# Performance work log

Hardware: AMD Instinct MI355X
Metric: run time of the kernel (lower is better)

Reference implementation:

```python
import jax, jax.numpy as jnp
import numpy as np

B, M, N = 16, 64, 64
F = 64
H2 = 2 * F
L = 2
OUT1, OUT2, PREDS = 32, 32, 256


def skew(x):
    # (b,m,n,c) -> (b,m,m+n-1,c); row i shifted right by i
    b, m, n, c = x.shape
    pad = jnp.pad(x, ((0, 0), (0, 0), (0, m - 1), (0, 0)))
    return jax.vmap(lambda row, r: jnp.roll(row, r, axis=1), in_axes=(1, 0), out_axes=1)(pad, jnp.arange(m))


def unskew(x):
    b, m, n2, c = x.shape
    n = n2 - m + 1
    un = jax.vmap(lambda row, r: jnp.roll(row, -r, axis=1), in_axes=(1, 0), out_axes=1)(x, jnp.arange(m))
    return un[:, :, :n]


def _ln(x, s, b, eps=1e-6):
    mu = jnp.mean(x, axis=-1, keepdims=True)
    var = jnp.mean(jnp.square(x - mu), axis=-1, keepdims=True)
    return (x - mu) * jax.lax.rsqrt(var + eps) * s + b


def _diag_layer(xin, lns, lnb, wis, bis, wss, bss, woc, boc, h0p):
    # xin: (b,m,n2,2F); scan over diagonals (n2 axis)
    b, m, n2, h2 = xin.shape
    f = h2 // 2

    def step(carry, xt):  # xt: (b,m,2F)
        h, c = carry
        xn = _ln(xt, lns, lnb)
        # is_kernel: 1x1 conv == linear; ss_kernel: causal k=2 conv along m
        hprev = jnp.pad(h, ((0, 0), (1, 0), (0, 0)))[:, :-1]
        z = xn @ wis + bis + hprev @ wss[0] + h @ wss[1] + bss  # (b,m,4F)
        fg, ig, og, gg = jnp.split(z, 4, axis=-1)
        cn = jax.nn.sigmoid(fg) * c + jax.nn.sigmoid(ig) * jnp.tanh(gg)
        hn = jax.nn.sigmoid(og) * jnp.tanh(cn)
        x_out = hn @ woc + boc + xn  # residual uses post-LN x (as in source)
        return (hn, cn), x_out

    h0t = jnp.broadcast_to(h0p, (b, m, f))  # h0p: (1,F)
    c0 = jnp.zeros((b, m, f), xin.dtype)
    _, out = jax.lax.scan(step, (h0t, c0), xin.transpose(2, 0, 1, 3))
    return out.transpose(1, 2, 0, 3)


def _forward(im, conv_in_k, conv_in_b, ln_s, ln_b, w_is, b_is, w_ss, b_ss,
             w_oc, b_oc, h0, w_out1, b_out1, w_out2, b_out2, w_head, b_head):
    # mask-A for the 7x7 input conv
    mask = jnp.ones(conv_in_k.shape, conv_in_k.dtype)
    mask = mask.at[3:, 4:].set(0.0)
    mask = mask.at[4:].set(0.0)
    mask = mask.at[3, 3].set(0.0)
    x = skew(im)  # (b,m,n2,1)
    x = jax.lax.conv_general_dilated(x, conv_in_k * mask, (1, 1), 'SAME',
                                     dimension_numbers=('NHWC', 'HWIO', 'NHWC')) + conv_in_b
    b, m, n2, h2 = x.shape
    for l in range(ln_s.shape[0]):
        left = _diag_layer(x, ln_s[l, 0], ln_b[l, 0], w_is[l, 0], b_is[l, 0],
                           w_ss[l, 0], b_ss[l, 0], w_oc[l, 0], b_oc[l, 0], h0[l, 0])
        right = _diag_layer(x[:, :, ::-1, :], ln_s[l, 1], ln_b[l, 1], w_is[l, 1], b_is[l, 1],
                            w_ss[l, 1], b_ss[l, 1], w_oc[l, 1], b_oc[l, 1], h0[l, 1])[:, :, ::-1, :]
        right = jnp.concatenate([jnp.zeros((b, 1, n2, h2), x.dtype), right[:, :-1]], axis=1)
        x = left + right
    x = unskew(x)  # (b,m,n,2F)
    x = x @ w_out1 + b_out1
    x = x @ w_out2 + b_out2
    return x @ w_head + b_head  # (b,m,n,256)


def setup_inputs() -> dict:
    key = jax.random.key(0)
    ks = jax.random.split(key, 10)
    rn = lambda k, s: jax.random.normal(k, s, jnp.float32) * 0.05
    return {
        "im": jax.random.uniform(ks[0], (B, M, N, 1), jnp.float32),
        "conv_in_k": rn(ks[1], (7, 7, 1, H2)),
        "conv_in_b": jnp.zeros((H2,), jnp.float32),
        "ln_s": jnp.ones((L, 2, H2), jnp.float32),
        "ln_b": jnp.zeros((L, 2, H2), jnp.float32),
        "w_is": rn(ks[2], (L, 2, H2, 4 * F)),
        "b_is": jnp.zeros((L, 2, 4 * F), jnp.float32),
        "w_ss": rn(ks[3], (L, 2, 2, F, 4 * F)),
        "b_ss": jnp.zeros((L, 2, 4 * F), jnp.float32),
        "w_oc": rn(ks[4], (L, 2, F, H2)),
        "b_oc": jnp.zeros((L, 2, H2), jnp.float32),
        "h0": rn(ks[5], (L, 2, 1, F)),
        "w_out1": rn(ks[6], (H2, OUT1)),
        "b_out1": jnp.zeros((OUT1,), jnp.float32),
        "w_out2": rn(ks[7], (OUT1, OUT2)),
        "b_out2": jnp.zeros((OUT2,), jnp.float32),
        "w_head": rn(ks[8], (OUT2, PREDS)),
        "b_head": jnp.zeros((PREDS,), jnp.float32),
    }


def reference(im, conv_in_k, conv_in_b, ln_s, ln_b, w_is, b_is, w_ss, b_ss,
              w_oc, b_oc, h0, w_out1, b_out1, w_out2, b_out2, w_head, b_head):
    return _forward(im, conv_in_k, conv_in_b, ln_s, ln_b, w_is, b_is, w_ss, b_ss,
                    w_oc, b_oc, h0, w_out1, b_out1, w_out2, b_out2, w_head, b_head)
```

## Files before the change

### kernel.cpp

```cpp
#include <hip/hip_runtime.h>

typedef unsigned short ushort_t;
typedef unsigned int uint_t;
typedef __attribute__((ext_vector_type(8))) short s8bf;
typedef __attribute__((ext_vector_type(4))) float f32x4;

#define N2 127
#define ACT ((size_t)16*64*127*128)
#define HNE ((size_t)16*64*127*64)
#define MBW ((size_t)32*3*127*64)

__device__ inline float bf_lo(uint_t v){ return __uint_as_float(v << 16); }
__device__ inline float bf_hi(uint_t v){ return __uint_as_float(v & 0xffff0000u); }
__device__ inline ushort_t f2bf(float f){
  uint_t u = __float_as_uint(f);
  uint_t r = ((u >> 16) & 1u) + 0x7fffu;
  return (ushort_t)((u + r) >> 16);
}
__device__ inline uint_t cvt_pk_bf16(float lo, float hi){
  uint_t r;
  asm("v_cvt_pk_bf16_f32 %0, %1, %2" : "=v"(r) : "v"(lo), "v"(hi));
  return r;
}
__device__ inline float bf2f(ushort_t h){ return __uint_as_float(((uint_t)h) << 16); }
__device__ inline float frcp(float x){ return __builtin_amdgcn_rcpf(x); }
__device__ inline float sigm(float x){ return frcp(1.f + __expf(-x)); }
__device__ inline float tanhf_(float x){
  float e = __expf(2.f * x);
  return 1.f - 2.f * frcp(1.f + e);
}
__device__ inline void unpack8(uint4 u, float* x){
  x[0]=bf_lo(u.x); x[1]=bf_hi(u.x); x[2]=bf_lo(u.y); x[3]=bf_hi(u.y);
  x[4]=bf_lo(u.z); x[5]=bf_hi(u.z); x[6]=bf_lo(u.w); x[7]=bf_hi(u.w);
}
__device__ inline f32x4 zero4(){ f32x4 v; v[0]=0.f; v[1]=0.f; v[2]=0.f; v[3]=0.f; return v; }
__device__ inline f32x4 splat4(float s){ f32x4 v; v[0]=s; v[1]=s; v[2]=s; v[3]=s; return v; }

__device__ inline void rowstats16(const float* xr, float& mu, float& rstd){
  float s0=0.f, q0=0.f;
#pragma unroll
  for (int k = 0; k < 16; k++){ s0 += xr[k]; q0 += xr[k]*xr[k]; }
  s0 += __shfl_xor(s0, 1); q0 += __shfl_xor(q0, 1);
  s0 += __shfl_xor(s0, 2); q0 += __shfl_xor(q0, 2);
  s0 += __shfl_xor(s0, 4); q0 += __shfl_xor(q0, 4);
  mu = s0 * 0.0078125f;
  float var = q0 * 0.0078125f - mu*mu;
  rstd = rsqrtf(var + 1e-6f);
}

__global__ __launch_bounds__(256) void prep_kernel(
    const float* __restrict__ im, const float* __restrict__ cb,
    const float* __restrict__ ck,
    const float* __restrict__ w_is, const float* __restrict__ w_ss,
    const float* __restrict__ b_is, const float* __restrict__ b_ss,
    const float* __restrict__ w_oc, const float* __restrict__ w1,
    const float* __restrict__ w2, const float* __restrict__ wh,
    ushort_t* __restrict__ out,
    ushort_t* __restrict__ zWp, ushort_t* __restrict__ wisp,
    ushort_t* __restrict__ wocp,
    float* __restrict__ zbias, float* __restrict__ w1T,
    float* __restrict__ w2T, float* __restrict__ whT,
    uint_t* __restrict__ mb)
{
  __shared__ float ims[4][64];
  const int tid = threadIdx.x;

  if (blockIdx.x < 1024){
    const int b = blockIdx.x >> 6;
    const int i = blockIdx.x & 63;
    {
      int r = tid >> 6, c = tid & 63;
      int ii = i - 3 + r;
      ims[r][c] = (ii >= 0) ? im[(b*64 + ii)*64 + c] : 0.f;
    }
    const int ch = tid & 127;
    const int jh = tid >> 7;
    float kwreg[24];
#pragma unroll
    for (int tau = 0; tau < 24; tau++){
      int di = (tau < 21) ? (tau/7 - 3) : 0;
      int dj = (tau < 21) ? (tau%7 - 3) : (tau - 24);
      kwreg[tau] = ck[((di+3)*7 + (dj+3))*128 + ch];
    }
    const float cbv = cb[ch];
    __syncthreads();
    ushort_t* orow = out + ((size_t)(b*64 + i)*N2)*128 + ch;
#pragma unroll 1
    for (int jt = 0; jt < 64; jt++){
      int j = jt*2 + jh;
      if (j >= N2) break;
      int base = j - i;
      float acc = cbv;
#pragma unroll
      for (int tau = 0; tau < 24; tau++){
        int di = (tau < 21) ? (tau/7 - 3) : 0;
        int dj = (tau < 21) ? (tau%7 - 3) : (tau - 24);
        int jx = base + dj - di;
        int r = di + 3;
        if (jx >= 0 && jx < 64)
          acc += ims[r][jx] * kwreg[tau];
      }
      orow[(size_t)j*128] = f2bf(acc);
    }
    return;
  }

  int idx = (blockIdx.x - 1024) * 256 + tid;
  if (idx < 131072){
    int ld = idx >> 15; int r = idx & 32767;
    int e = r & 7, lane = (r >> 3) & 63, ctg = (r >> 9) & 15, kk = r >> 13;
    int k = kk*32 + ((lane >> 4) & 3)*8 + e;
    int n = ctg*16 + (lane & 15);
    float v;
    if (k < 64) v = w_ss[(((size_t)ld*2 + 0)*64 + k)*256 + n];
    else        v = w_ss[(((size_t)ld*2 + 1)*64 + (k-64))*256 + n];
    zWp[idx] = f2bf(v);
  } else if (idx < 262144){
    int r0 = idx - 131072;
    int ld = r0 >> 15; int r = r0 & 32767;
    int e = r & 7, lane = (r >> 3) & 63, ctg = (r >> 9) & 15, kk = r >> 13;
    int k = kk*32 + ((lane >> 4) & 3)*8 + e;
    int n = ctg*16 + (lane & 15);
    wisp[r0] = f2bf(w_is[((size_t)ld*128 + k)*256 + n]);
  } else if (idx < 294912){
    int r0 = idx - 262144;
    int ld = r0 >> 13; int r = r0 & 8191;
    int e = r & 7, lane = (r >> 3) & 63, ctg = (r >> 9) & 7, kk = (r >> 12) & 1;
    int k = kk*32 + ((lane >> 4) & 3)*8 + e;
    int n = ctg*16 + (lane & 15);
    wocp[r0] = f2bf(w_oc[((size_t)ld*64 + k)*128 + n]);
  } else if (idx < 295936){
    int r = idx - 294912;
    zbias[r] = b_is[r] + b_ss[r];
  } else if (idx < 300032){
    int r = idx - 295936;
    int c = r >> 7, k = r & 127;
    w1T[r] = w1[k*32 + c];
  } else if (idx < 301056){
    int r = idx - 300032;
    int c = r >> 5, k = r & 31;
    w2T[r] = w2[k*32 + c];
  } else if (idx < 309248){
    int r = idx - 301056;
    int o = r >> 5, k = r & 31;
    whT[r] = wh[k*256 + o];
  } else if (idx >= 312320 && idx < (int)(312320 + MBW/4)){
    ((uint4*)mb)[idx - 312320] = make_uint4(0u, 0u, 0u, 0u);
  }
}

__device__ inline void write_frags512(const ushort_t* __restrict__ XN,
                                      ushort_t* __restrict__ dst, int tid){
  int lane = tid & 63, t8 = tid >> 6;
  int quad = (lane >> 4) & 3, l16 = lane & 15;
  int kk = t8 >> 1, rh = (t8 & 1)*2;
#pragma unroll
  for (int i = 0; i < 2; i++){
    int rt = rh + i;
    uint4 v = *(const uint4*)&XN[(size_t)(rt*16 + l16)*136 + kk*32 + quad*8];
    *(uint4*)(dst + (size_t)((kk*4 + rt)*64 + lane)*8) = v;
  }
}

__device__ inline void ln_to_XN16(ushort_t* __restrict__ XN, int row, int lq,
                                  const float* xr, float mu, float rstd,
                                  const float* __restrict__ ln_s,
                                  const float* __restrict__ ln_b, int ld){
  uint_t o[8];
#pragma unroll
  for (int k2 = 0; k2 < 8; k2++){
    int c = lq*16 + 2*k2;
    float a = (xr[2*k2]   - mu)*rstd*ln_s[ld*128 + c]     + ln_b[ld*128 + c];
    float b = (xr[2*k2+1] - mu)*rstd*ln_s[ld*128 + c + 1] + ln_b[ld*128 + c + 1];
    o[k2] = cvt_pk_bf16(a, b);
  }
  uint4* dst = (uint4*)&XN[(size_t)row*136 + lq*16];
  dst[0] = make_uint4(o[0], o[1], o[2], o[3]);
  dst[1] = make_uint4(o[4], o[5], o[6], o[7]);
}

__global__ __launch_bounds__(512) void stage0_kernel(
    int lnlyr, const ushort_t* __restrict__ Xbuf,
    const float* __restrict__ ln_s, const float* __restrict__ ln_b,
    ushort_t* __restrict__ xnfL, ushort_t* __restrict__ xnfR)
{
  __shared__ __align__(16) ushort_t XN[64*136];

  const int tid = threadIdx.x;
  const int bj = blockIdx.x;
  const int b = bj / 127, j = bj - b*127;
  const int row = tid >> 3, lq = tid & 7;

  float xr[16];
  {
    const uint4* p = (const uint4*)(Xbuf + ((size_t)(b*64 + row)*N2 + j)*128 + lq*16);
    unpack8(p[0], xr); unpack8(p[1], xr+8);
  }
  float mu, rstd;
  rowstats16(xr, mu, rstd);

  ln_to_XN16(XN, row, lq, xr, mu, rstd, ln_s, ln_b, lnlyr*2 + 0);
  __syncthreads();
  write_frags512(XN, xnfL + (size_t)bj*8192, tid);
  __syncthreads();
  ln_to_XN16(XN, row, lq, xr, mu, rstd, ln_s, ln_b, lnlyr*2 + 1);
  __syncthreads();
  write_frags512(XN, xnfR + (size_t)bj*8192, tid);
}

__global__ __launch_bounds__(512, 1) void stage12_kernel(
    int mode, int woclyr, int lnlyr,
    ushort_t* __restrict__ Xbuf,
    const ushort_t* __restrict__ hnL, const ushort_t* __restrict__ hnR,
    const ushort_t* __restrict__ wocp, const float* __restrict__ b_oc,
    const float* __restrict__ ln_s, const float* __restrict__ ln_b,
    ushort_t* __restrict__ xnfL, ushort_t* __restrict__ xnfR)
{
  __shared__ __align__(16) float Xout[64*132];
  __shared__ __align__(16) ushort_t XN[64*136];
  __shared__ __align__(16) ushort_t XNh[64*72];

  const int tid = threadIdx.x;
  const int bj = blockIdx.x;
  const int b = bj / 127, j = bj - b*127;
  const int w8 = tid >> 6;
  const int lane = tid & 63, quad = (lane >> 4) & 3, l16 = lane & 15;
  const int row = tid >> 3, lq = tid & 7;

  float xr[16];
  {
    const uint4* p = (const uint4*)(Xbuf + ((size_t)(b*64 + row)*N2 + j)*128 + lq*16);
    unpack8(p[0], xr); unpack8(p[1], xr+8);
  }
  float mu, rstd;
  rowstats16(xr, mu, rstd);

#pragma unroll 1
  for (int s = 0; s < 2; s++){
    const int ld = woclyr*2 + s;
    ln_to_XN16(XN, row, lq, xr, mu, rstd, ln_s, ln_b, ld);
    {
      const ushort_t* hp = s ? hnR : hnL;
      const uint4* p = (const uint4*)(hp + ((size_t)(b*64 + row)*N2 + j)*64 + lq*8);
      *(uint4*)&XNh[(size_t)row*72 + lq*8] = p[0];
    }
    __syncthreads();
    s8bf bw[2];
#pragma unroll
    for (int kk = 0; kk < 2; kk++)
      bw[kk] = *(const s8bf*)(wocp + (size_t)ld*8192 + (size_t)(((kk*8 + w8)*64 + lane)*8));
    f32x4 a2[4];
#pragma unroll
    for (int rt = 0; rt < 4; rt++) a2[rt] = zero4();
#pragma unroll
    for (int kk = 0; kk < 2; kk++)
#pragma unroll
      for (int rt = 0; rt < 4; rt++){
        s8bf a = *(const s8bf*)&XNh[(size_t)(rt*16 + l16)*72 + kk*32 + quad*8];
        a2[rt] = __builtin_amdgcn_mfma_f32_16x16x32_bf16(a, bw[kk], a2[rt], 0, 0, 0);
      }
    const float bv = b_oc[ld*128 + w8*16 + l16];
    const int col = w8*16 + l16;
#pragma unroll
    for (int rt = 0; rt < 4; rt++)
#pragma unroll
      for (int r = 0; r < 4; r++){
        int rr = rt*16 + quad*4 + r;
        float v = a2[rt][r] + bv + bf2f(XN[(size_t)rr*136 + col]);
        if (s == 0) Xout[(size_t)rr*132 + col] = v;
        else if (rr < 63) Xout[(size_t)(rr + 1)*132 + col] += v;
      }
    __syncthreads();
  }

  float xo[16];
#pragma unroll
  for (int k = 0; k < 16; k++) xo[k] = Xout[(size_t)row*132 + lq*16 + k];
  {
    uint_t o[8];
#pragma unroll
    for (int k = 0; k < 8; k++) o[k] = cvt_pk_bf16(xo[2*k], xo[2*k + 1]);
    uint4* dst = (uint4*)(Xbuf + ((size_t)(b*64 + row)*N2 + j)*128 + lq*16);
    dst[0] = make_uint4(o[0], o[1], o[2], o[3]);
    dst[1] = make_uint4(o[4], o[5], o[6], o[7]);
  }
  if (mode == 2) return;

  float mu2, rstd2;
  rowstats16(xo, mu2, rstd2);
  ln_to_XN16(XN, row, lq, xo, mu2, rstd2, ln_s, ln_b, lnlyr*2 + 0);
  __syncthreads();
  write_frags512(XN, xnfL + (size_t)bj*8192, tid);
  __syncthreads();
  ln_to_XN16(XN, row, lq, xo, mu2, rstd2, ln_s, ln_b, lnlyr*2 + 1);
  __syncthreads();
  write_frags512(XN, xnfR + (size_t)bj*8192, tid);
}

__global__ __launch_bounds__(256, 1) void diag_kernel(
    const ushort_t* __restrict__ xnfL, const ushort_t* __restrict__ xnfR,
    ushort_t* __restrict__ hnL, ushort_t* __restrict__ hnR,
    const ushort_t* __restrict__ zWp, const ushort_t* __restrict__ wisp,
    const float* __restrict__ zbias, const float* __restrict__ h0, int layer,
    uint_t* __restrict__ mb)
{
  __shared__ ushort_t A[2][16][136];

  const int tid = threadIdx.x;
  const int g = blockIdx.x & 3;
  const int b = (blockIdx.x >> 2) & 15;
  const int d = blockIdx.x >> 6;
  const int ld = layer*2 + d;
  const ushort_t* xnf = d ? xnfR : xnfL;
  ushort_t* hp = d ? hnR : hnL;

  const int w = tid >> 6;
  const int lane = tid & 63;
  const int quad = lane >> 4;
  const int l16 = lane & 15;
  const int cg = w*16 + l16;

  s8bf bss[4][4], bis[4][4];
#pragma unroll
  for (int kk = 0; kk < 4; kk++)
#pragma unroll
    for (int ct = 0; ct < 4; ct++){
      size_t fo = (size_t)(((kk*16 + (w + 4*ct))*64 + lane)*8);
      bss[kk][ct] = *(const s8bf*)(zWp  + (size_t)ld*32768 + fo);
      bis[kk][ct] = *(const s8bf*)(wisp + (size_t)ld*32768 + fo);
    }
  float zb[4];
#pragma unroll
  for (int ct = 0; ct < 4; ct++) zb[ct] = zbias[ld*256 + ct*64 + cg];

  float c_reg[4] = {0.f, 0.f, 0.f, 0.f};

  {
    int r2 = tid >> 4, q8 = tid & 15;
    const float* h0p = h0 + ld*64;
#pragma unroll
    for (int k = 0; k < 8; k++){
      int c = q8*8 + k;
      ushort_t hb = f2bf(h0p[c & 63]);
      ushort_t v;
      if (c < 64) v = (g == 0 && r2 == 0) ? (ushort_t)0 : hb;
      else        v = hb;
      A[0][r2][c] = v;
      A[1][r2][c] = v;
    }
  }

  const int stp8 = d ? -8192 : 8192;
  const ushort_t* xbase = xnf + ((size_t)b*127 + (d ? 126 : 0))*8192;
  uint4 xf[4];
#pragma unroll
  for (int kk = 0; kk < 4; kk++)
    xf[kk] = *(const uint4*)(xbase + (size_t)((kk*4 + g)*64 + lane)*8);

  f32x4 acc[4];
#pragma unroll
  for (int ct = 0; ct < 4; ct++) acc[ct] = splat4(zb[ct]);
#pragma unroll
  for (int kk = 0; kk < 4; kk++){
    s8bf a = *(const s8bf*)&xf[kk];
#pragma unroll
    for (int ct = 0; ct < 4; ct++)
      acc[ct] = __builtin_amdgcn_mfma_f32_16x16x32_bf16(a, bis[kk][ct], acc[ct], 0, 0, 0);
  }
  const ushort_t* pfp = xbase + stp8;
#pragma unroll
  for (int kk = 0; kk < 4; kk++)
    xf[kk] = *(const uint4*)(pfp + (size_t)((kk*4 + g)*64 + lane)*8);
  pfp += stp8;

  const int dj64 = d ? -64 : 64;
  ushort_t* hlane = hp + ((size_t)(b*64 + g*16 + quad*4)*N2 + (d ? 126 : 0))*64 + cg;

  const int bd = b*2 + d;
  uint_t* mbOut = mb + ((size_t)(bd*3 + g)*127)*64;
  const uint_t* mbIn = mb + ((size_t)(bd*3 + (g > 0 ? g - 1 : 0))*127)*64;
  const uint_t stampBase = (uint_t)layer * 127u;
  const bool isProd = (g < 3);
  const bool isCons = (g > 0) && (w == 1);

  __syncthreads();

#pragma unroll 1
  for (int t = 0; t < 127; t++){
    const int pr = t & 1, pn = pr ^ 1;
    const uint_t stamp = stampBase + (uint_t)t + 1u;
    const bool doFetch = isCons && (t < 126);

    uint_t pv = 0;
    if (doFetch)
      pv = __hip_atomic_load(mbIn + (size_t)t*64 + lane,
                             __ATOMIC_RELAXED, __HIP_MEMORY_SCOPE_AGENT);

#pragma unroll
    for (int kk = 0; kk < 4; kk++){
      s8bf af = *(const s8bf*)&A[pr][l16][kk*32 + quad*8];
#pragma unroll
      for (int ct = 0; ct < 4; ct++)
        acc[ct] = __builtin_amdgcn_mfma_f32_16x16x32_bf16(af, bss[kk][ct], acc[ct], 0, 0, 0);
    }

#pragma unroll
    for (int r = 0; r < 4; r++){
      float fg = sigm(acc[0][r]);
      float ig = sigm(acc[1][r]);
      float og = sigm(acc[2][r]);
      float gg = tanhf_(acc[3][r]);
      float cn = fg*c_reg[r] + ig*gg;
      c_reg[r] = cn;
      float hn = og * tanhf_(cn);
      int rr = quad*4 + r;
      ushort_t hb = f2bf(hn);
      A[pn][rr][64 + cg] = hb;
      if (rr < 15) A[pn][rr + 1][cg] = hb;
      hlane[(size_t)r*8128] = hb;
      if (r == 3 && isProd && quad == 3 && t < 126)
        __hip_atomic_store(mbOut + (size_t)t*64 + cg,
                           (stamp << 16) | (uint_t)hb,
                           __ATOMIC_RELAXED, __HIP_MEMORY_SCOPE_AGENT);
    }
    hlane += dj64;

    if (t < 126){
#pragma unroll
      for (int ct = 0; ct < 4; ct++) acc[ct] = splat4(zb[ct]);
#pragma unroll
      for (int kk = 0; kk < 4; kk++){
        s8bf a = *(const s8bf*)&xf[kk];
#pragma unroll
        for (int ct = 0; ct < 4; ct++)
          acc[ct] = __builtin_amdgcn_mfma_f32_16x16x32_bf16(a, bis[kk][ct], acc[ct], 0, 0, 0);
      }
      if (t < 125){
#pragma unroll
        for (int kk = 0; kk < 4; kk++)
          xf[kk] = *(const uint4*)(pfp + (size_t)((kk*4 + g)*64 + lane)*8);
        pfp += stp8;
      }
    }

    if (doFetch){
      while (!__all((pv >> 16) == stamp))
        pv = __hip_atomic_load(mbIn + (size_t)t*64 + lane,
                               __ATOMIC_RELAXED, __HIP_MEMORY_SCOPE_AGENT);
      A[pn][0][lane] = (ushort_t)(pv & 0xffffu);
    }

    __syncthreads();
  }
}

__global__ __launch_bounds__(512) void head_kernel(
    const ushort_t* __restrict__ xfin,
    const float* __restrict__ w1T, const float* __restrict__ b1,
    const float* __restrict__ w2T, const float* __restrict__ b2,
    const float* __restrict__ whT, const float* __restrict__ bh,
    float* __restrict__ out)
{
  __shared__ float xf[64][132];
  __shared__ float v1[64][36];
  __shared__ float v2[64][36];
  int tid = threadIdx.x;
  int b = blockIdx.x >> 6, i = blockIdx.x & 63;
  {
    int jj = tid >> 3, q = tid & 7;
    size_t base = ((size_t)(b*64 + i)*N2 + (i + jj))*128 + q*16;
    const uint4* pL = (const uint4*)(xfin + base);
    float x[16];
    unpack8(pL[0], x); unpack8(pL[1], x+8);
#pragma unroll
    for (int k = 0; k < 16; k++) xf[jj][q*16 + k] = x[k];
  }
  __syncthreads();
  {
    int c1 = tid & 31, jg = tid >> 5;
    float accv[4];
#pragma unroll
    for (int q = 0; q < 4; q++) accv[q] = b1[c1];
#pragma unroll 1
    for (int kc = 0; kc < 4; kc++){
      float wr[32];
      const float4* wp = (const float4*)(w1T + c1*128 + kc*32);
#pragma unroll
      for (int kk = 0; kk < 8; kk++) ((float4*)wr)[kk] = wp[kk];
#pragma unroll
      for (int jj2 = 0; jj2 < 4; jj2++){
        int jr = jg*4 + jj2;
        float a0=0.f,a1=0.f,a2=0.f,a3=0.f;
#pragma unroll
        for (int kk = 0; kk < 8; kk++){
          float4 xv = *(const float4*)&xf[jr][kc*32 + kk*4];
          a0 += xv.x*wr[kk*4]; a1 += xv.y*wr[kk*4+1]; a2 += xv.z*wr[kk*4+2]; a3 += xv.w*wr[kk*4+3];
        }
        accv[jj2] += (a0+a1)+(a2+a3);
      }
    }
#pragma unroll
    for (int jj2 = 0; jj2 < 4; jj2++) v1[jg*4 + jj2][c1] = accv[jj2];
  }
  __syncthreads();
  {
    int c2 = tid & 31, jg = tid >> 5;
    float wr[32];
    const float4* wp = (const float4*)(w2T + c2*32);
#pragma unroll
    for (int kk = 0; kk < 8; kk++) ((float4*)wr)[kk] = wp[kk];
#pragma unroll
    for (int jj2 = 0; jj2 < 4; jj2++){
      int jr = jg*4 + jj2;
      float a0=0.f,a1=0.f,a2=0.f,a3=0.f;
#pragma unroll
      for (int kk = 0; kk < 8; kk++){
        float4 xv = *(const float4*)&v1[jr][kk*4];
        a0 += xv.x*wr[kk*4]; a1 += xv.y*wr[kk*4+1]; a2 += xv.z*wr[kk*4+2]; a3 += xv.w*wr[kk*4+3];
      }
      v2[jr][c2] = b2[c2] + (a0+a1)+(a2+a3);
    }
  }
  __syncthreads();
  {
    int o = tid & 255, jh = tid >> 8;
    float wr[32];
    const float4* wp = (const float4*)(whT + o*32);
#pragma unroll
    for (int kk = 0; kk < 8; kk++) ((float4*)wr)[kk] = wp[kk];
    float bo = bh[o];
#pragma unroll 1
    for (int jr2 = 0; jr2 < 32; jr2++){
      int jr = jh*32 + jr2;
      float a0=0.f,a1=0.f,a2=0.f,a3=0.f;
#pragma unroll
      for (int kk = 0; kk < 8; kk++){
        float4 xv = *(const float4*)&v2[jr][kk*4];
        a0 += xv.x*wr[kk*4]; a1 += xv.y*wr[kk*4+1]; a2 += xv.z*wr[kk*4+2]; a3 += xv.w*wr[kk*4+3];
      }
      out[(((size_t)b*64 + i)*64 + jr)*256 + o] = bo + (a0+a1)+(a2+a3);
    }
  }
}

extern "C" void kernel_launch(void* const* d_in, const int* in_sizes, int n_in,
                              void* d_out, int out_size, void* d_ws, size_t ws_size,
                              hipStream_t stream)
{
  const float* im   = (const float*)d_in[0];
  const float* ck   = (const float*)d_in[1];
  const float* cb   = (const float*)d_in[2];
  const float* ln_s = (const float*)d_in[3];
  const float* ln_b = (const float*)d_in[4];
  const float* w_is = (const float*)d_in[5];
  const float* b_is = (const float*)d_in[6];
  const float* w_ss = (const float*)d_in[7];
  const float* b_ss = (const float*)d_in[8];
  const float* w_oc = (const float*)d_in[9];
  const float* b_oc = (const float*)d_in[10];
  const float* h0   = (const float*)d_in[11];
  const float* w1   = (const float*)d_in[12];
  const float* b1   = (const float*)d_in[13];
  const float* w2   = (const float*)d_in[14];
  const float* b2   = (const float*)d_in[15];
  const float* wh   = (const float*)d_in[16];
  const float* bh   = (const float*)d_in[17];

  ushort_t* Xbuf = (ushort_t*)d_ws;
  ushort_t* xnfL = Xbuf + ACT;
  ushort_t* xnfR = xnfL + ACT;
  ushort_t* hnL  = xnfR + ACT;
  ushort_t* hnR  = hnL + HNE;
  ushort_t* zWp  = hnR + HNE;
  ushort_t* wisp = zWp + 131072;
  ushort_t* wocp = wisp + 131072;
  float* zbias = (float*)(wocp + 32768);
  float* w1T   = zbias + 1024;
  float* w2T   = w1T + 4096;
  float* whT   = w2T + 1024;
  uint_t* mb   = (uint_t*)d_out;

  prep_kernel<<<3006, 256, 0, stream>>>(im, cb, ck, w_is, w_ss, b_is, b_ss,
                                        w_oc, w1, w2, wh, Xbuf,
                                        zWp, wisp, wocp, zbias, w1T, w2T, whT, mb);
  stage0_kernel<<<2032, 512, 0, stream>>>(0, Xbuf, ln_s, ln_b, xnfL, xnfR);
  diag_kernel<<<128, 256, 0, stream>>>(xnfL, xnfR, hnL, hnR, zWp, wisp, zbias, h0, 0, mb);
  stage12_kernel<<<2032, 512, 0, stream>>>(1, 0, 1, Xbuf, hnL, hnR,
                                           wocp, b_oc, ln_s, ln_b, xnfL, xnfR);
  diag_kernel<<<128, 256, 0, stream>>>(xnfL, xnfR, hnL, hnR, zWp, wisp, zbias, h0, 1, mb);
  stage12_kernel<<<2032, 512, 0, stream>>>(2, 1, 0, Xbuf, hnL, hnR,
                                           wocp, b_oc, ln_s, ln_b, xnfL, xnfR);
  head_kernel<<<1024, 512, 0, stream>>>(Xbuf, w1T, b1, w2T, b2, whT, bh, (float*)d_out);
}
```

Baseline: 655.0 us.

## Fuse stage and diagonal kernels with per-column flags to overlap producer and scan

Merges the LN/fragment producer kernels with the diagonal LSTM scan kernel into single launches. The first 128 blocks run the scan and spin on per-(batch,diagonal) flags that producer blocks set after writing fragments with agent-scope stores. The aim is to overlap the serial diagonal scan with the parallel stage work and cut kernel launch gaps. It risks deadlock if the scan blocks occupy CUs the producers need, adds spin-wait overhead, and doubles the hn buffers so layer-0 outputs stay intact while layer 1 runs.

```diff
diff --git a/kernel.cpp b/kernel.cpp
--- a/kernel.cpp
+++ b/kernel.cpp
@@ -60,7 +60,7 @@
     ushort_t* __restrict__ wocp,
     float* __restrict__ zbias, float* __restrict__ w1T,
     float* __restrict__ w2T, float* __restrict__ whT,
-    uint_t* __restrict__ mb)
+    uint_t* __restrict__ flg, uint_t* __restrict__ mb)
 {
   __shared__ float ims[4][64];
   const int tid = threadIdx.x;
@@ -144,8 +144,27 @@
     int r = idx - 301056;
     int o = r >> 5, k = r & 31;
     whT[r] = wh[k*256 + o];
+  } else if (idx < 311280){
+    flg[idx - 309248] = 0u;
   } else if (idx >= 312320 && idx < (int)(312320 + MBW/4)){
     ((uint4*)mb)[idx - 312320] = make_uint4(0u, 0u, 0u, 0u);
+  }
+}
+
+__device__ inline void write_frags512A(const ushort_t* __restrict__ XN,
+                                       ushort_t* __restrict__ dst, int tid){
+  int lane = tid & 63, t8 = tid >> 6;
+  int quad = (lane >> 4) & 3, l16 = lane & 15;
+  int kk = t8 >> 1, rh = (t8 & 1)*2;
+#pragma unroll
+  for (int i = 0; i < 2; i++){
+    int rt = rh + i;
+    uint4 v = *(const uint4*)&XN[(size_t)(rt*16 + l16)*136 + kk*32 + quad*8];
+    uint_t* d = (uint_t*)(dst + (size_t)((kk*4 + rt)*64 + lane)*8);
+    __hip_atomic_store(d+0, v.x, __ATOMIC_RELAXED, __HIP_MEMORY_SCOPE_AGENT);
+    __hip_atomic_store(d+1, v.y, __ATOMIC_RELAXED, __HIP_MEMORY_SCOPE_AGENT);
+    __hip_atomic_store(d+2, v.z, __ATOMIC_RELAXED, __HIP_MEMORY_SCOPE_AGENT);
+    __hip_atomic_store(d+3, v.w, __ATOMIC_RELAXED, __HIP_MEMORY_SCOPE_AGENT);
   }
 }
 
@@ -179,15 +198,12 @@
   dst[1] = make_uint4(o[4], o[5], o[6], o[7]);
 }
 
-__global__ __launch_bounds__(512) void stage0_kernel(
-    int lnlyr, const ushort_t* __restrict__ Xbuf,
+__device__ void stage0_body(int bj, int tid, const ushort_t* __restrict__ Xbuf,
     const float* __restrict__ ln_s, const float* __restrict__ ln_b,
-    ushort_t* __restrict__ xnfL, ushort_t* __restrict__ xnfR)
-{
-  __shared__ __align__(16) ushort_t XN[64*136];
-
-  const int tid = threadIdx.x;
-  const int bj = blockIdx.x;
+    ushort_t* __restrict__ xnfL, ushort_t* __restrict__ xnfR,
+    uint_t* __restrict__ flg, uint_t fstamp, char* smem)
+{
+  ushort_t* XN = (ushort_t*)smem;
   const int b = bj / 127, j = bj - b*127;
   const int row = tid >> 3, lq = tid & 7;
 
@@ -199,29 +215,31 @@
   float mu, rstd;
   rowstats16(xr, mu, rstd);
 
-  ln_to_XN16(XN, row, lq, xr, mu, rstd, ln_s, ln_b, lnlyr*2 + 0);
-  __syncthreads();
-  write_frags512(XN, xnfL + (size_t)bj*8192, tid);
-  __syncthreads();
-  ln_to_XN16(XN, row, lq, xr, mu, rstd, ln_s, ln_b, lnlyr*2 + 1);
-  __syncthreads();
-  write_frags512(XN, xnfR + (size_t)bj*8192, tid);
-}
-
-__global__ __launch_bounds__(512, 1) void stage12_kernel(
-    int mode, int woclyr, int lnlyr,
+  ln_to_XN16(XN, row, lq, xr, mu, rstd, ln_s, ln_b, 0);
+  __syncthreads();
+  write_frags512A(XN, xnfL + (size_t)bj*8192, tid);
+  __syncthreads();
+  ln_to_XN16(XN, row, lq, xr, mu, rstd, ln_s, ln_b, 1);
+  __syncthreads();
+  write_frags512A(XN, xnfR + (size_t)bj*8192, tid);
+  asm volatile("s_waitcnt vmcnt(0)" ::: "memory");
+  __syncthreads();
+  if (tid == 0)
+    __hip_atomic_store(&flg[bj], fstamp, __ATOMIC_RELAXED, __HIP_MEMORY_SCOPE_AGENT);
+}
+
+__device__ void stage12_body(int bj, int tid, int mode, int woclyr, int lnlyr,
     ushort_t* __restrict__ Xbuf,
     const ushort_t* __restrict__ hnL, const ushort_t* __restrict__ hnR,
     const ushort_t* __restrict__ wocp, const float* __restrict__ b_oc,
     const float* __restrict__ ln_s, const float* __restrict__ ln_b,
-    ushort_t* __restrict__ xnfL, ushort_t* __restrict__ xnfR)
-{
-  __shared__ __align__(16) float Xout[64*132];
-  __shared__ __align__(16) ushort_t XN[64*136];
-  __shared__ __align__(16) ushort_t XNh[64*72];
-
-  const int tid = threadIdx.x;
-  const int bj = blockIdx.x;
+    ushort_t* __restrict__ xnfL, ushort_t* __restrict__ xnfR,
+    uint_t* __restrict__ flg, uint_t fstamp, char* smem)
+{
+  float* Xout  = (float*)smem;
+  ushort_t* XN = (ushort_t*)(smem + 33792);
+  ushort_t* XNh= (ushort_t*)(smem + 51200);
+
   const int b = bj / 127, j = bj - b*127;
   const int w8 = tid >> 6;
   const int lane = tid & 63, quad = (lane >> 4) & 3, l16 = lane & 15;
@@ -290,26 +308,28 @@
   rowstats16(xo, mu2, rstd2);
   ln_to_XN16(XN, row, lq, xo, mu2, rstd2, ln_s, ln_b, lnlyr*2 + 0);
   __syncthreads();
-  write_frags512(XN, xnfL + (size_t)bj*8192, tid);
+  write_frags512A(XN, xnfL + (size_t)bj*8192, tid);
   __syncthreads();
   ln_to_XN16(XN, row, lq, xo, mu2, rstd2, ln_s, ln_b, lnlyr*2 + 1);
   __syncthreads();
-  write_frags512(XN, xnfR + (size_t)bj*8192, tid);
-}
-
-__global__ __launch_bounds__(256, 1) void diag_kernel(
+  write_frags512A(XN, xnfR + (size_t)bj*8192, tid);
+  asm volatile("s_waitcnt vmcnt(0)" ::: "memory");
+  __syncthreads();
+  if (tid == 0)
+    __hip_atomic_store(&flg[bj], fstamp, __ATOMIC_RELAXED, __HIP_MEMORY_SCOPE_AGENT);
+}
+
+__device__ void diag_body(int blk, int tid,
     const ushort_t* __restrict__ xnfL, const ushort_t* __restrict__ xnfR,
     ushort_t* __restrict__ hnL, ushort_t* __restrict__ hnR,
     const ushort_t* __restrict__ zWp, const ushort_t* __restrict__ wisp,
     const float* __restrict__ zbias, const float* __restrict__ h0, int layer,
-    uint_t* __restrict__ mb)
-{
-  __shared__ ushort_t A[2][16][136];
-
-  const int tid = threadIdx.x;
-  const int g = blockIdx.x & 3;
-  const int b = (blockIdx.x >> 2) & 15;
-  const int d = blockIdx.x >> 6;
+    uint_t* __restrict__ mb, const uint_t* __restrict__ flg, uint_t fstamp,
+    ushort_t* __restrict__ Ap )
+{
+  const int g = blk & 3;
+  const int b = (blk >> 2) & 15;
+  const int d = blk >> 6;
   const int ld = layer*2 + d;
   const ushort_t* xnf = d ? xnfR : xnfL;
   ushort_t* hp = d ? hnR : hnL;
@@ -345,13 +365,20 @@
       ushort_t v;
       if (c < 64) v = (g == 0 && r2 == 0) ? (ushort_t)0 : hb;
       else        v = hb;
-      A[0][r2][c] = v;
-      A[1][r2][c] = v;
+      Ap[(0*16 + r2)*136 + c] = v;
+      Ap[(1*16 + r2)*136 + c] = v;
     }
   }
 
   const int stp8 = d ? -8192 : 8192;
   const ushort_t* xbase = xnf + ((size_t)b*127 + (d ? 126 : 0))*8192;
+  const uint_t* fbase = flg + b*127;
+
+  {
+    const uint_t* f0 = fbase + (d ? 126 : 0);
+    while (__hip_atomic_load(f0, __ATOMIC_RELAXED, __HIP_MEMORY_SCOPE_AGENT) < fstamp) {}
+    asm volatile("" ::: "memory");
+  }
   uint4 xf[4];
 #pragma unroll
   for (int kk = 0; kk < 4; kk++)
@@ -366,12 +393,19 @@
 #pragma unroll
     for (int ct = 0; ct < 4; ct++)
       acc[ct] = __builtin_amdgcn_mfma_f32_16x16x32_bf16(a, bis[kk][ct], acc[ct], 0, 0, 0);
+  }
+  {
+    const uint_t* f1 = fbase + (d ? 125 : 1);
+    while (__hip_atomic_load(f1, __ATOMIC_RELAXED, __HIP_MEMORY_SCOPE_AGENT) < fstamp) {}
+    asm volatile("" ::: "memory");
   }
   const ushort_t* pfp = xbase + stp8;
 #pragma unroll
   for (int kk = 0; kk < 4; kk++)
     xf[kk] = *(const uint4*)(pfp + (size_t)((kk*4 + g)*64 + lane)*8);
   pfp += stp8;
+  const uint_t* fpf = fbase + (d ? 124 : 2);
+  const int fstep = d ? -1 : 1;
 
   const int dj64 = d ? -64 : 64;
   ushort_t* hlane = hp + ((size_t)(b*64 + g*16 + quad*4)*N2 + (d ? 126 : 0))*64 + cg;
@@ -395,10 +429,13 @@
     if (doFetch)
       pv = __hip_atomic_load(mbIn + (size_t)t*64 + lane,
                              __ATOMIC_RELAXED, __HIP_MEMORY_SCOPE_AGENT);
+    uint_t fv = 0xffffffffu;
+    if (t < 125)
+      fv = __hip_atomic_load(fpf, __ATOMIC_RELAXED, __HIP_MEMORY_SCOPE_AGENT);
 
 #pragma unroll
     for (int kk = 0; kk < 4; kk++){
-      s8bf af = *(const s8bf*)&A[pr][l16][kk*32 + quad*8];
+      s8bf af = *(const s8bf*)&Ap[(pr*16 + l16)*136 + kk*32 + quad*8];
 #pragma unroll
       for (int ct = 0; ct < 4; ct++)
         acc[ct] = __builtin_amdgcn_mfma_f32_16x16x32_bf16(af, bss[kk][ct], acc[ct], 0, 0, 0);
@@ -415,8 +452,8 @@
       float hn = og * tanhf_(cn);
       int rr = quad*4 + r;
       ushort_t hb = f2bf(hn);
-      A[pn][rr][64 + cg] = hb;
-      if (rr < 15) A[pn][rr + 1][cg] = hb;
+      Ap[(pn*16 + rr)*136 + 64 + cg] = hb;
+      if (rr < 15) Ap[(pn*16 + rr + 1)*136 + cg] = hb;
       hlane[(size_t)r*8128] = hb;
       if (r == 3 && isProd && quad == 3 && t < 126)
         __hip_atomic_store(mbOut + (size_t)t*64 + cg,
@@ -436,10 +473,15 @@
           acc[ct] = __builtin_amdgcn_mfma_f32_16x16x32_bf16(a, bis[kk][ct], acc[ct], 0, 0, 0);
       }
       if (t < 125){
+        if (fv < fstamp){
+          while (__hip_atomic_load(fpf, __ATOMIC_RELAXED, __HIP_MEMORY_SCOPE_AGENT) < fstamp) {}
+        }
+        asm volatile("" ::: "memory");
 #pragma unroll
         for (int kk = 0; kk < 4; kk++)
           xf[kk] = *(const uint4*)(pfp + (size_t)((kk*4 + g)*64 + lane)*8);
         pfp += stp8;
+        fpf += fstep;
       }
     }
 
@@ -447,11 +489,72 @@
       while (!__all((pv >> 16) == stamp))
         pv = __hip_atomic_load(mbIn + (size_t)t*64 + lane,
                                __ATOMIC_RELAXED, __HIP_MEMORY_SCOPE_AGENT);
-      A[pn][0][lane] = (ushort_t)(pv & 0xffffu);
+      Ap[(pn*16 + 0)*136 + lane] = (ushort_t)(pv & 0xffffu);
     }
 
     __syncthreads();
   }
+}
+
+__global__ __launch_bounds__(512, 1) void sd0_kernel(
+    ushort_t* __restrict__ Xbuf,
+    const float* __restrict__ ln_s, const float* __restrict__ ln_b,
+    ushort_t* __restrict__ xnfL, ushort_t* __restrict__ xnfR,
+    ushort_t* __restrict__ hnL, ushort_t* __restrict__ hnR,
+    const ushort_t* __restrict__ zWp, const ushort_t* __restrict__ wisp,
+    const float* __restrict__ zbias, const float* __restrict__ h0,
+    uint_t* __restrict__ mb, uint_t* __restrict__ flg)
+{
+  __shared__ __align__(16) char smem[17408];
+  if (blockIdx.x < 128){
+    if (threadIdx.x >= 256){
+#pragma unroll 1
+      for (int t = 0; t < 128; t++) __syncthreads();
+      return;
+    }
+    diag_body(blockIdx.x, threadIdx.x, xnfL, xnfR, hnL, hnR, zWp, wisp,
+              zbias, h0, 0, mb, flg, 1u, (ushort_t*)smem);
+    return;
+  }
+  stage0_body(blockIdx.x - 128, threadIdx.x, Xbuf, ln_s, ln_b,
+              xnfL, xnfR, flg, 1u, smem);
+}
+
+__global__ __launch_bounds__(512, 1) void sd1_kernel(
+    ushort_t* __restrict__ Xbuf,
+    const ushort_t* __restrict__ hn0L, const ushort_t* __restrict__ hn0R,
+    const ushort_t* __restrict__ wocp, const float* __restrict__ b_oc,
+    const float* __restrict__ ln_s, const float* __restrict__ ln_b,
+    ushort_t* __restrict__ xnfL, ushort_t* __restrict__ xnfR,
+    ushort_t* __restrict__ hn1L, ushort_t* __restrict__ hn1R,
+    const ushort_t* __restrict__ zWp, const ushort_t* __restrict__ wisp,
+    const float* __restrict__ zbias, const float* __restrict__ h0,
+    uint_t* __restrict__ mb, uint_t* __restrict__ flg)
+{
+  __shared__ __align__(16) char smem[60416];
+  if (blockIdx.x < 128){
+    if (threadIdx.x >= 256){
+#pragma unroll 1
+      for (int t = 0; t < 128; t++) __syncthreads();
+      return;
+    }
+    diag_body(blockIdx.x, threadIdx.x, xnfL, xnfR, hn1L, hn1R, zWp, wisp,
+              zbias, h0, 1, mb, flg, 2u, (ushort_t*)smem);
+    return;
+  }
+  stage12_body(blockIdx.x - 128, threadIdx.x, 1, 0, 1, Xbuf, hn0L, hn0R,
+               wocp, b_oc, ln_s, ln_b, xnfL, xnfR, flg, 2u, smem);
+}
+
+__global__ __launch_bounds__(512, 1) void stage2_kernel(
+    ushort_t* __restrict__ Xbuf,
+    const ushort_t* __restrict__ hnL, const ushort_t* __restrict__ hnR,
+    const ushort_t* __restrict__ wocp, const float* __restrict__ b_oc,
+    const float* __restrict__ ln_s, const float* __restrict__ ln_b)
+{
+  __shared__ __align__(16) char smem[60416];
+  stage12_body(blockIdx.x, threadIdx.x, 2, 1, 0, Xbuf, hnL, hnR,
+               wocp, b_oc, ln_s, ln_b, nullptr, nullptr, nullptr, 0u, smem);
 }
 
 __global__ __launch_bounds__(512) void head_kernel(
@@ -569,26 +672,29 @@
   ushort_t* Xbuf = (ushort_t*)d_ws;
   ushort_t* xnfL = Xbuf + ACT;
   ushort_t* xnfR = xnfL + ACT;
-  ushort_t* hnL  = xnfR + ACT;
-  ushort_t* hnR  = hnL + HNE;
-  ushort_t* zWp  = hnR + HNE;
+  ushort_t* hn0L = xnfR + ACT;
+  ushort_t* hn0R = hn0L + HNE;
+  ushort_t* hn1L = hn0R + HNE;
+  ushort_t* hn1R = hn1L + HNE;
+  ushort_t* zWp  = hn1R + HNE;
   ushort_t* wisp = zWp + 131072;
   ushort_t* wocp = wisp + 131072;
   float* zbias = (float*)(wocp + 32768);
   float* w1T   = zbias + 1024;
   float* w2T   = w1T + 4096;
   float* whT   = w2T + 1024;
+  uint_t* flg  = (uint_t*)(whT + 8192);
   uint_t* mb   = (uint_t*)d_out;
 
   prep_kernel<<<3006, 256, 0, stream>>>(im, cb, ck, w_is, w_ss, b_is, b_ss,
                                         w_oc, w1, w2, wh, Xbuf,
-                                        zWp, wisp, wocp, zbias, w1T, w2T, whT, mb);
-  stage0_kernel<<<2032, 512, 0, stream>>>(0, Xbuf, ln_s, ln_b, xnfL, xnfR);
-  diag_kernel<<<128, 256, 0, stream>>>(xnfL, xnfR, hnL, hnR, zWp, wisp, zbias, h0, 0, mb);
-  stage12_kernel<<<2032, 512, 0, stream>>>(1, 0, 1, Xbuf, hnL, hnR,
-                                           wocp, b_oc, ln_s, ln_b, xnfL, xnfR);
-  diag_kernel<<<128, 256, 0, stream>>>(xnfL, xnfR, hnL, hnR, zWp, wisp, zbias, h0, 1, mb);
-  stage12_kernel<<<2032, 512, 0, stream>>>(2, 1, 0, Xbuf, hnL, hnR,
-                                           wocp, b_oc, ln_s, ln_b, xnfL, xnfR);
+                                        zWp, wisp, wocp, zbias, w1T, w2T, whT,
+                                        flg, mb);
+  sd0_kernel<<<2160, 512, 0, stream>>>(Xbuf, ln_s, ln_b, xnfL, xnfR,
+                                       hn0L, hn0R, zWp, wisp, zbias, h0, mb, flg);
+  sd1_kernel<<<2160, 512, 0, stream>>>(Xbuf, hn0L, hn0R, wocp, b_oc, ln_s, ln_b,
+                                       xnfL, xnfR, hn1L, hn1R, zWp, wisp,
+                                       zbias, h0, mb, flg);
+  stage2_kernel<<<2032, 512, 0, stream>>>(Xbuf, hn1L, hn1R, wocp, b_oc, ln_s, ln_b);
   head_kernel<<<1024, 512, 0, stream>>>(Xbuf, w1T, b1, w2T, b2, whT, bh, (float*)d_out);
 }
```

Measured after the change: 1.079 ms. +64.7%, slower.
